# Performance work log

Measured on AMD Instinct MI355X. Metric: run time of the kernel, lower is better.

Reference implementation:

```python
import jax, jax.numpy as jnp
import numpy as np

N = 27            # hardcoded node count in the module
D = 1024          # state_dim
E = D * 5         # MHA embed dim = 5120
H = 4             # n_heads


def setup_inputs() -> dict:
    key = jax.random.key(0)
    ks = jax.random.split(key, 6)
    s = 0.02
    return {
        "node_states": jax.random.normal(ks[0], (N, D, 5), jnp.float32),
        "hist_prev": jax.random.normal(ks[1], (N, D, 5), jnp.float32),
        "granger_w": jax.random.normal(ks[2], (1, 2 * E), jnp.float32) * s,
        "granger_b": jnp.zeros((1,), jnp.float32),
        "in_proj_w": jax.random.normal(ks[3], (3 * E, E), jnp.float32) * s,
        "in_proj_b": jnp.zeros((3 * E,), jnp.float32),
        "out_proj_w": jax.random.normal(ks[4], (E, E), jnp.float32) * s,
        "out_proj_b": jnp.zeros((E,), jnp.float32),
        "light_hertz": 500,
    }


def _mha(x, in_w, in_b, out_w, out_b):
    # x: [N, E]; torch MultiheadAttention with q=k=v=x, batch of 1
    qkv = x @ in_w.T + in_b                       # [N, 3E]
    q, k, v = jnp.split(qkv, 3, axis=-1)          # each [N, E]
    hd = E // H
    q = q.reshape(N, H, hd).transpose(1, 0, 2)    # [H, N, hd]
    k = k.reshape(N, H, hd).transpose(1, 0, 2)
    v = v.reshape(N, H, hd).transpose(1, 0, 2)
    scores = jnp.einsum('hqd,hkd->hqk', q, k) / jnp.sqrt(jnp.float32(hd))
    attn = jax.nn.softmax(scores, axis=-1)        # [H, N, N]
    o = jnp.einsum('hqk,hkd->hqd', attn, v)       # [H, N, hd]
    o = o.transpose(1, 0, 2).reshape(N, E)
    return o @ out_w.T + out_b                    # [N, E]


def reference(node_states, hist_prev, granger_w, granger_b,
              in_proj_w, in_proj_b, out_proj_w, out_proj_b, light_hertz):
    node_flat = node_states.reshape(N, E)         # [N, E]
    hist_flat = hist_prev.reshape(N, E)           # [N, E]

    # Granger pairwise test, vectorized: pred_input = [hist[j], node[i]]
    # score[i, j] = sigmoid(hist[j] . w_h + node[i] . w_n + b)
    w_h = granger_w[0, :E]
    w_n = granger_w[0, E:]
    col = node_flat @ w_n                          # [N] -> varies with i
    row = hist_flat @ w_h                          # [N] -> varies with j
    adj = jax.nn.sigmoid(col[:, None] + row[None, :] + granger_b[0])  # [N, N]
    causal_adj = adj * (1.0 - jnp.eye(N, dtype=adj.dtype))            # zero diagonal

    hertz_weight = jnp.clip(jnp.float32(light_hertz) / 1000.0, 0.1, 1.0)
    attended = _mha(node_flat, in_proj_w, in_proj_b, out_proj_w, out_proj_b)
    out = (attended * hertz_weight).reshape(N, D, 5)
    return out, causal_adj
```

## Files before the change

kernel.cpp:

```cpp
#include <hip/hip_runtime.h>

#define NROW 27
#define EDIM 5120
#define QKVDIM 15360
#define HD 1280

typedef __attribute__((ext_vector_type(8))) short bf16x8;
typedef __attribute__((ext_vector_type(4))) float f32x4;

__device__ inline short f2bf(float x) {
    unsigned u = __builtin_bit_cast(unsigned, x);
    u = (u + 0x7FFFu + ((u >> 16) & 1u)) >> 16;
    return (short)u;
}
__device__ inline float bf2f(short h) {
    unsigned u = ((unsigned)(unsigned short)h) << 16;
    return __builtin_bit_cast(float, u);
}

#define KC 64
#define LDK 72

__device__ inline void loadX2(float* xbuf, const float* xp, bool xok) {
    if (xok) {
        *(float4*)&xbuf[0] = ((const float4*)xp)[0];
        *(float4*)&xbuf[4] = ((const float4*)xp)[1];
    } else {
        #pragma unroll
        for (int j = 0; j < 8; ++j) xbuf[j] = 0.f;
    }
}

__device__ inline void loadWfrag(float4* wreg, const float* wp0, const float* wp1) {
    #pragma unroll
    for (int s = 0; s < 2; ++s) {
        wreg[s * 2 + 0] = *(const float4*)(wp0 + 32 * s);
        wreg[s * 2 + 1] = *(const float4*)(wp0 + 32 * s + 4);
        wreg[4 + s * 2 + 0] = *(const float4*)(wp1 + 32 * s);
        wreg[4 + s * 2 + 1] = *(const float4*)(wp1 + 32 * s + 4);
    }
}

__global__ __launch_bounds__(256, 3)
void gemm_regw(const float* __restrict__ X, const float* __restrict__ W,
               float* __restrict__ Cp, int K, int Ntot, int Kblk)
{
    __shared__ __align__(16) short Xhi[2][32][LDK];
    __shared__ __align__(16) short Xlo[2][32][LDK];

    const int tid = threadIdx.x;
    const int n0 = blockIdx.x * 128;
    const int k0 = blockIdx.y * Kblk;

    const int lane = tid & 63;
    const int wv   = tid >> 6;
    const int lm   = lane & 15;
    const int q8   = (lane >> 4) * 8;

    f32x4 acc[2][2] = {};

    const int xr = tid >> 3;
    const int xk = (tid & 7) * 8;
    const bool xok = (xr < NROW);
    const float* xp = X + (size_t)(xok ? xr : 0) * K + k0 + xk;

    const float* wp0 = W + (size_t)(n0 + 32 * wv + lm) * K + k0 + q8;
    const float* wp1 = wp0 + (size_t)16 * K;

    float  xbuf[8];
    float4 wreg[8];

    loadX2(xbuf, xp, xok);
    loadWfrag(wreg, wp0, wp1);

    const int nc = Kblk / KC;
    int p = 0;
    for (int c = 0; c < nc; ++c) {
        {
            bf16x8 h8, l8;
            #pragma unroll
            for (int j = 0; j < 8; ++j) {
                short h = f2bf(xbuf[j]);
                h8[j] = h;
                l8[j] = f2bf(xbuf[j] - bf2f(h));
            }
            *(bf16x8*)&Xhi[p][xr][xk] = h8;
            *(bf16x8*)&Xlo[p][xr][xk] = l8;
        }

        bf16x8 whi[2][2], wlo[2][2];
        #pragma unroll
        for (int g = 0; g < 2; ++g) {
            #pragma unroll
            for (int s = 0; s < 2; ++s) {
                const float4 a = wreg[g * 4 + s * 2 + 0];
                const float4 b = wreg[g * 4 + s * 2 + 1];
                const float f[8] = {a.x, a.y, a.z, a.w, b.x, b.y, b.z, b.w};
                bf16x8 h8, l8;
                #pragma unroll
                for (int j = 0; j < 8; ++j) {
                    short h = f2bf(f[j]);
                    h8[j] = h;
                    l8[j] = f2bf(f[j] - bf2f(h));
                }
                whi[s][g] = h8;
                wlo[s][g] = l8;
            }
        }

        if (c + 1 < nc) {
            xp  += KC;
            wp0 += KC;
            wp1 += KC;
            loadX2(xbuf, xp, xok);
            loadWfrag(wreg, wp0, wp1);
        }

        __syncthreads();

        #pragma unroll
        for (int s = 0; s < 2; ++s) {
            const int ko = 32 * s + q8;
            bf16x8 ah0 = *(const bf16x8*)&Xhi[p][lm][ko];
            bf16x8 ah1 = *(const bf16x8*)&Xhi[p][lm + 16][ko];
            bf16x8 al0 = *(const bf16x8*)&Xlo[p][lm][ko];
            bf16x8 al1 = *(const bf16x8*)&Xlo[p][lm + 16][ko];

            acc[0][0] = __builtin_amdgcn_mfma_f32_16x16x32_bf16(ah0, whi[s][0], acc[0][0], 0, 0, 0);
            acc[0][0] = __builtin_amdgcn_mfma_f32_16x16x32_bf16(ah0, wlo[s][0], acc[0][0], 0, 0, 0);
            acc[0][0] = __builtin_amdgcn_mfma_f32_16x16x32_bf16(al0, whi[s][0], acc[0][0], 0, 0, 0);

            acc[0][1] = __builtin_amdgcn_mfma_f32_16x16x32_bf16(ah0, whi[s][1], acc[0][1], 0, 0, 0);
            acc[0][1] = __builtin_amdgcn_mfma_f32_16x16x32_bf16(ah0, wlo[s][1], acc[0][1], 0, 0, 0);
            acc[0][1] = __builtin_amdgcn_mfma_f32_16x16x32_bf16(al0, whi[s][1], acc[0][1], 0, 0, 0);

            acc[1][0] = __builtin_amdgcn_mfma_f32_16x16x32_bf16(ah1, whi[s][0], acc[1][0], 0, 0, 0);
            acc[1][0] = __builtin_amdgcn_mfma_f32_16x16x32_bf16(ah1, wlo[s][0], acc[1][0], 0, 0, 0);
            acc[1][0] = __builtin_amdgcn_mfma_f32_16x16x32_bf16(al1, whi[s][0], acc[1][0], 0, 0, 0);

            acc[1][1] = __builtin_amdgcn_mfma_f32_16x16x32_bf16(ah1, whi[s][1], acc[1][1], 0, 0, 0);
            acc[1][1] = __builtin_amdgcn_mfma_f32_16x16x32_bf16(ah1, wlo[s][1], acc[1][1], 0, 0, 0);
            acc[1][1] = __builtin_amdgcn_mfma_f32_16x16x32_bf16(al1, whi[s][1], acc[1][1], 0, 0, 0);
        }
        p ^= 1;
    }

    const size_t base = (size_t)blockIdx.y * NROW * Ntot;
    #pragma unroll
    for (int mi = 0; mi < 2; ++mi) {
        #pragma unroll
        for (int r = 0; r < 4; ++r) {
            const int m = mi * 16 + (lane >> 4) * 4 + r;
            if (m < NROW) {
                #pragma unroll
                for (int ni = 0; ni < 2; ++ni) {
                    const int n = n0 + 32 * wv + ni * 16 + lm;
                    Cp[base + (size_t)m * Ntot + n] = acc[mi][ni][r];
                }
            }
        }
    }
}

__global__ __launch_bounds__(256)
void reduce_kernel(const float* __restrict__ Cp, const float* __restrict__ bias,
                   float* __restrict__ out, int Ntot, int nky, const int* __restrict__ hz,
                   const float* __restrict__ cr, const float* __restrict__ gb,
                   float* __restrict__ adj)
{
    if (adj && blockIdx.x == gridDim.x - 1) {
        for (int t = threadIdx.x; t < NROW * NROW; t += 256) {
            const int i = t / NROW, j = t % NROW;
            float v = 0.f;
            if (i != j) {
                float z = cr[i] + cr[NROW + j] + gb[0];
                v = 1.0f / (1.0f + expf(-z));
            }
            adj[t] = v;
        }
        return;
    }
    const int idx = blockIdx.x * 256 + threadIdx.x;
    const int total4 = NROW * Ntot / 4;
    if (idx >= total4) return;
    float4 s = ((const float4*)Cp)[idx];
    for (int k = 1; k < nky; ++k) {
        float4 p = ((const float4*)(Cp + (size_t)k * NROW * Ntot))[idx];
        s.x += p.x; s.y += p.y; s.z += p.z; s.w += p.w;
    }
    const int n = (idx * 4) % Ntot;
    float4 b = *(const float4*)(bias + n);
    s.x += b.x; s.y += b.y; s.z += b.z; s.w += b.w;
    if (hz) {
        float h = (float)hz[0] * 0.001f;
        float sc = fminf(fmaxf(h, 0.1f), 1.0f);
        s.x *= sc; s.y *= sc; s.z *= sc; s.w *= sc;
    }
    ((float4*)out)[idx] = s;
}

__global__ __launch_bounds__(256)
void colrow_kernel(const float* __restrict__ node, const float* __restrict__ hist,
                   const float* __restrict__ gw, float* __restrict__ cr)
{
    const int b = blockIdx.x;
    const float* x = (b < NROW) ? node + (size_t)b * EDIM : hist + (size_t)(b - NROW) * EDIM;
    const float* w = (b < NROW) ? gw + EDIM : gw;
    const int tid = threadIdx.x;
    float a = 0.f;
    for (int f = tid; f < EDIM / 4; f += 256) {
        float4 xv = ((const float4*)x)[f];
        float4 wv = ((const float4*)w)[f];
        a += xv.x * wv.x + xv.y * wv.y + xv.z * wv.z + xv.w * wv.w;
    }
    #pragma unroll
    for (int off = 32; off; off >>= 1) a += __shfl_down(a, off);
    __shared__ float red[4];
    if ((tid & 63) == 0) red[tid >> 6] = a;
    __syncthreads();
    if (tid == 0) cr[b] = red[0] + red[1] + red[2] + red[3];
}

__global__ __launch_bounds__(256)
void attn_kernel(const float* __restrict__ qkv, float* __restrict__ O)
{
    __shared__ float qs[HD];
    __shared__ float sc[NROW];
    __shared__ float pr[NROW];
    const int bx = blockIdx.x;
    const int h = bx & 3;
    const int i = bx >> 2;
    const int tid = threadIdx.x;

    const size_t qoff = (size_t)i * QKVDIM + (size_t)h * HD;
    for (int d = tid; d < HD; d += 256) qs[d] = qkv[qoff + d];
    __syncthreads();

    const int wid = tid >> 6, lane = tid & 63;
    for (int j = wid; j < NROW; j += 4) {
        const float* kr = qkv + (size_t)j * QKVDIM + EDIM + (size_t)h * HD;
        float a = 0.f;
        #pragma unroll
        for (int it = 0; it < 5; ++it) {
            int d4 = lane + 64 * it;
            float4 k4 = *(const float4*)(kr + 4 * d4);
            float4 q4 = *(const float4*)(qs + 4 * d4);
            a += q4.x * k4.x + q4.y * k4.y + q4.z * k4.z + q4.w * k4.w;
        }
        #pragma unroll
        for (int off = 32; off; off >>= 1) a += __shfl_down(a, off);
        if (lane == 0) sc[j] = a * 0.02795084971874737f;
    }
    __syncthreads();

    float mxv = -1e30f;
    for (int j = 0; j < NROW; ++j) mxv = fmaxf(mxv, sc[j]);
    float s = 0.f;
    for (int j = 0; j < NROW; ++j) s += expf(sc[j] - mxv);
    if (tid < NROW) pr[tid] = expf(sc[tid] - mxv) / s;
    __syncthreads();

    for (int d4 = tid; d4 < HD / 4; d4 += 256) {
        float4 o = make_float4(0.f, 0.f, 0.f, 0.f);
        for (int j = 0; j < NROW; ++j) {
            const float4 v4 = *(const float4*)(qkv + (size_t)j * QKVDIM + 2 * EDIM + (size_t)h * HD + 4 * d4);
            const float p = pr[j];
            o.x = fmaf(p, v4.x, o.x);
            o.y = fmaf(p, v4.y, o.y);
            o.z = fmaf(p, v4.z, o.z);
            o.w = fmaf(p, v4.w, o.w);
        }
        *(float4*)(O + (size_t)i * EDIM + (size_t)h * HD + 4 * d4) = o;
    }
}

extern "C" void kernel_launch(void* const* d_in, const int* in_sizes, int n_in,
                              void* d_out, int out_size, void* d_ws, size_t ws_size,
                              hipStream_t stream)
{
    const float* node = (const float*)d_in[0];
    const float* hist = (const float*)d_in[1];
    const float* gw   = (const float*)d_in[2];
    const float* gb   = (const float*)d_in[3];
    const float* inw  = (const float*)d_in[4];
    const float* inb  = (const float*)d_in[5];
    const float* outw = (const float*)d_in[6];
    const float* outb = (const float*)d_in[7];
    const int*   hz   = (const int*)d_in[8];

    float* out = (float*)d_out;

    float* Cp1  = (float*)d_ws;
    float* qkvf = Cp1 + (size_t)8 * NROW * QKVDIM;
    float* Obuf = qkvf + (size_t)NROW * QKVDIM;
    float* Cp2  = Obuf + (size_t)NROW * EDIM;
    float* cr   = Cp2 + (size_t)16 * NROW * EDIM;

    colrow_kernel<<<54, 256, 0, stream>>>(node, hist, gw, cr);

    gemm_regw<<<dim3(120, 8), 256, 0, stream>>>(node, inw, Cp1, EDIM, QKVDIM, EDIM / 8);
    reduce_kernel<<<NROW * QKVDIM / 4 / 256, 256, 0, stream>>>(
        Cp1, inb, qkvf, QKVDIM, 8, nullptr, nullptr, nullptr, nullptr);

    attn_kernel<<<108, 256, 0, stream>>>(qkvf, Obuf);

    gemm_regw<<<dim3(40, 16), 256, 0, stream>>>(Obuf, outw, Cp2, EDIM, EDIM, EDIM / 16);
    reduce_kernel<<<NROW * EDIM / 4 / 256 + 1, 256, 0, stream>>>(
        Cp2, outb, out, EDIM, 16, hz, cr, gb, out + (size_t)NROW * EDIM);
}
```

Baseline: 534.5 us.

## Pre-split activations into bf16 hi/lo in producers and drop GEMM LDS staging

```diff
diff --git a/kernel.cpp b/kernel.cpp
--- a/kernel.cpp
+++ b/kernel.cpp
@@ -19,35 +19,86 @@
 }
 
 #define KC 64
-#define LDK 72
-
-__device__ inline void loadX2(float* xbuf, const float* xp, bool xok) {
-    if (xok) {
-        *(float4*)&xbuf[0] = ((const float4*)xp)[0];
-        *(float4*)&xbuf[4] = ((const float4*)xp)[1];
-    } else {
+
+__device__ __forceinline__ void loadW8(float4* wb, const float* wq0, const float* wq1) {
+    #pragma unroll
+    for (int s = 0; s < 2; ++s) {
+        wb[s * 2 + 0]     = *(const float4*)(wq0 + 32 * s);
+        wb[s * 2 + 1]     = *(const float4*)(wq0 + 32 * s + 4);
+        wb[4 + s * 2 + 0] = *(const float4*)(wq1 + 32 * s);
+        wb[4 + s * 2 + 1] = *(const float4*)(wq1 + 32 * s + 4);
+    }
+}
+
+__device__ __forceinline__ void gstep(
+    const short* __restrict__ xh0, const short* __restrict__ xh1,
+    const short* __restrict__ xl0, const short* __restrict__ xl1, bool xok1,
+    const float* __restrict__ wq0, const float* __restrict__ wq1,
+    int c, int nc, float4* wcur, float4* wnxt, f32x4 (&acc)[2][2])
+{
+    const int ko = c * KC;
+
+    bf16x8 ah0[2], ah1[2], al0[2], al1[2];
+    #pragma unroll
+    for (int s = 0; s < 2; ++s) {
+        ah0[s] = *(const bf16x8*)(xh0 + ko + 32 * s);
+        al0[s] = *(const bf16x8*)(xl0 + ko + 32 * s);
+        bf16x8 h1 = {}, l1 = {};
+        if (xok1) {
+            h1 = *(const bf16x8*)(xh1 + ko + 32 * s);
+            l1 = *(const bf16x8*)(xl1 + ko + 32 * s);
+        }
+        ah1[s] = h1;
+        al1[s] = l1;
+    }
+
+    if (c + 1 < nc) loadW8(wnxt, wq0 + (c + 1) * KC, wq1 + (c + 1) * KC);
+
+    bf16x8 whi[2][2], wlo[2][2];
+    #pragma unroll
+    for (int g = 0; g < 2; ++g) {
         #pragma unroll
-        for (int j = 0; j < 8; ++j) xbuf[j] = 0.f;
-    }
-}
-
-__device__ inline void loadWfrag(float4* wreg, const float* wp0, const float* wp1) {
+        for (int s = 0; s < 2; ++s) {
+            const float4 a = wcur[g * 4 + s * 2 + 0];
+            const float4 b = wcur[g * 4 + s * 2 + 1];
+            const float f[8] = {a.x, a.y, a.z, a.w, b.x, b.y, b.z, b.w};
+            bf16x8 h8, l8;
+            #pragma unroll
+            for (int j = 0; j < 8; ++j) {
+                short h = f2bf(f[j]);
+                h8[j] = h;
+                l8[j] = f2bf(f[j] - bf2f(h));
+            }
+            whi[s][g] = h8;
+            wlo[s][g] = l8;
+        }
+    }
+
     #pragma unroll
     for (int s = 0; s < 2; ++s) {
-        wreg[s * 2 + 0] = *(const float4*)(wp0 + 32 * s);
-        wreg[s * 2 + 1] = *(const float4*)(wp0 + 32 * s + 4);
-        wreg[4 + s * 2 + 0] = *(const float4*)(wp1 + 32 * s);
-        wreg[4 + s * 2 + 1] = *(const float4*)(wp1 + 32 * s + 4);
-    }
-}
-
-__global__ __launch_bounds__(256, 3)
-void gemm_regw(const float* __restrict__ X, const float* __restrict__ W,
-               float* __restrict__ Cp, int K, int Ntot, int Kblk)
-{
-    __shared__ __align__(16) short Xhi[2][32][LDK];
-    __shared__ __align__(16) short Xlo[2][32][LDK];
-
+        acc[0][0] = __builtin_amdgcn_mfma_f32_16x16x32_bf16(ah0[s], whi[s][0], acc[0][0], 0, 0, 0);
+        acc[0][0] = __builtin_amdgcn_mfma_f32_16x16x32_bf16(ah0[s], wlo[s][0], acc[0][0], 0, 0, 0);
+        acc[0][0] = __builtin_amdgcn_mfma_f32_16x16x32_bf16(al0[s], whi[s][0], acc[0][0], 0, 0, 0);
+
+        acc[0][1] = __builtin_amdgcn_mfma_f32_16x16x32_bf16(ah0[s], whi[s][1], acc[0][1], 0, 0, 0);
+        acc[0][1] = __builtin_amdgcn_mfma_f32_16x16x32_bf16(ah0[s], wlo[s][1], acc[0][1], 0, 0, 0);
+        acc[0][1] = __builtin_amdgcn_mfma_f32_16x16x32_bf16(al0[s], whi[s][1], acc[0][1], 0, 0, 0);
+
+        acc[1][0] = __builtin_amdgcn_mfma_f32_16x16x32_bf16(ah1[s], whi[s][0], acc[1][0], 0, 0, 0);
+        acc[1][0] = __builtin_amdgcn_mfma_f32_16x16x32_bf16(ah1[s], wlo[s][0], acc[1][0], 0, 0, 0);
+        acc[1][0] = __builtin_amdgcn_mfma_f32_16x16x32_bf16(al1[s], whi[s][0], acc[1][0], 0, 0, 0);
+
+        acc[1][1] = __builtin_amdgcn_mfma_f32_16x16x32_bf16(ah1[s], whi[s][1], acc[1][1], 0, 0, 0);
+        acc[1][1] = __builtin_amdgcn_mfma_f32_16x16x32_bf16(ah1[s], wlo[s][1], acc[1][1], 0, 0, 0);
+        acc[1][1] = __builtin_amdgcn_mfma_f32_16x16x32_bf16(al1[s], whi[s][1], acc[1][1], 0, 0, 0);
+    }
+}
+
+__global__ __launch_bounds__(256, 2)
+void gemm_regw(const short* __restrict__ Xhi, const short* __restrict__ Xlo,
+               const float* __restrict__ W, float* __restrict__ Cp,
+               int K, int Ntot, int Kblk)
+{
     const int tid = threadIdx.x;
     const int n0 = blockIdx.x * 128;
     const int k0 = blockIdx.y * Kblk;
@@ -59,90 +110,27 @@
 
     f32x4 acc[2][2] = {};
 
-    const int xr = tid >> 3;
-    const int xk = (tid & 7) * 8;
-    const bool xok = (xr < NROW);
-    const float* xp = X + (size_t)(xok ? xr : 0) * K + k0 + xk;
-
     const float* wp0 = W + (size_t)(n0 + 32 * wv + lm) * K + k0 + q8;
     const float* wp1 = wp0 + (size_t)16 * K;
 
-    float  xbuf[8];
-    float4 wreg[8];
-
-    loadX2(xbuf, xp, xok);
-    loadWfrag(wreg, wp0, wp1);
+    const bool xok1 = (lm + 16) < NROW;
+    const int  r1   = xok1 ? lm + 16 : 0;
+    const short* xh0 = Xhi + (size_t)lm * K + k0 + q8;
+    const short* xl0 = Xlo + (size_t)lm * K + k0 + q8;
+    const short* xh1 = Xhi + (size_t)r1 * K + k0 + q8;
+    const short* xl1 = Xlo + (size_t)r1 * K + k0 + q8;
+
+    float4 wA[8], wB[8];
+    loadW8(wA, wp0, wp1);
 
     const int nc = Kblk / KC;
-    int p = 0;
-    for (int c = 0; c < nc; ++c) {
-        {
-            bf16x8 h8, l8;
-            #pragma unroll
-            for (int j = 0; j < 8; ++j) {
-                short h = f2bf(xbuf[j]);
-                h8[j] = h;
-                l8[j] = f2bf(xbuf[j] - bf2f(h));
-            }
-            *(bf16x8*)&Xhi[p][xr][xk] = h8;
-            *(bf16x8*)&Xlo[p][xr][xk] = l8;
-        }
-
-        bf16x8 whi[2][2], wlo[2][2];
-        #pragma unroll
-        for (int g = 0; g < 2; ++g) {
-            #pragma unroll
-            for (int s = 0; s < 2; ++s) {
-                const float4 a = wreg[g * 4 + s * 2 + 0];
-                const float4 b = wreg[g * 4 + s * 2 + 1];
-                const float f[8] = {a.x, a.y, a.z, a.w, b.x, b.y, b.z, b.w};
-                bf16x8 h8, l8;
-                #pragma unroll
-                for (int j = 0; j < 8; ++j) {
-                    short h = f2bf(f[j]);
-                    h8[j] = h;
-                    l8[j] = f2bf(f[j] - bf2f(h));
-                }
-                whi[s][g] = h8;
-                wlo[s][g] = l8;
-            }
-        }
-
-        if (c + 1 < nc) {
-            xp  += KC;
-            wp0 += KC;
-            wp1 += KC;
-            loadX2(xbuf, xp, xok);
-            loadWfrag(wreg, wp0, wp1);
-        }
-
-        __syncthreads();
-
-        #pragma unroll
-        for (int s = 0; s < 2; ++s) {
-            const int ko = 32 * s + q8;
-            bf16x8 ah0 = *(const bf16x8*)&Xhi[p][lm][ko];
-            bf16x8 ah1 = *(const bf16x8*)&Xhi[p][lm + 16][ko];
-            bf16x8 al0 = *(const bf16x8*)&Xlo[p][lm][ko];
-            bf16x8 al1 = *(const bf16x8*)&Xlo[p][lm + 16][ko];
-
-            acc[0][0] = __builtin_amdgcn_mfma_f32_16x16x32_bf16(ah0, whi[s][0], acc[0][0], 0, 0, 0);
-            acc[0][0] = __builtin_amdgcn_mfma_f32_16x16x32_bf16(ah0, wlo[s][0], acc[0][0], 0, 0, 0);
-            acc[0][0] = __builtin_amdgcn_mfma_f32_16x16x32_bf16(al0, whi[s][0], acc[0][0], 0, 0, 0);
-
-            acc[0][1] = __builtin_amdgcn_mfma_f32_16x16x32_bf16(ah0, whi[s][1], acc[0][1], 0, 0, 0);
-            acc[0][1] = __builtin_amdgcn_mfma_f32_16x16x32_bf16(ah0, wlo[s][1], acc[0][1], 0, 0, 0);
-            acc[0][1] = __builtin_amdgcn_mfma_f32_16x16x32_bf16(al0, whi[s][1], acc[0][1], 0, 0, 0);
-
-            acc[1][0] = __builtin_amdgcn_mfma_f32_16x16x32_bf16(ah1, whi[s][0], acc[1][0], 0, 0, 0);
-            acc[1][0] = __builtin_amdgcn_mfma_f32_16x16x32_bf16(ah1, wlo[s][0], acc[1][0], 0, 0, 0);
-            acc[1][0] = __builtin_amdgcn_mfma_f32_16x16x32_bf16(al1, whi[s][0], acc[1][0], 0, 0, 0);
-
-            acc[1][1] = __builtin_amdgcn_mfma_f32_16x16x32_bf16(ah1, whi[s][1], acc[1][1], 0, 0, 0);
-            acc[1][1] = __builtin_amdgcn_mfma_f32_16x16x32_bf16(ah1, wlo[s][1], acc[1][1], 0, 0, 0);
-            acc[1][1] = __builtin_amdgcn_mfma_f32_16x16x32_bf16(al1, whi[s][1], acc[1][1], 0, 0, 0);
-        }
-        p ^= 1;
+    int c = 0;
+    while (c < nc) {
+        gstep(xh0, xh1, xl0, xl1, xok1, wp0, wp1, c, nc, wA, wB, acc);
+        ++c;
+        if (c >= nc) break;
+        gstep(xh0, xh1, xl0, xl1, xok1, wp0, wp1, c, nc, wB, wA, acc);
+        ++c;
     }
 
     const size_t base = (size_t)blockIdx.y * NROW * Ntot;
@@ -201,17 +189,28 @@
 
 __global__ __launch_bounds__(256)
 void colrow_kernel(const float* __restrict__ node, const float* __restrict__ hist,
-                   const float* __restrict__ gw, float* __restrict__ cr)
+                   const float* __restrict__ gw, float* __restrict__ cr,
+                   short* __restrict__ XhiG, short* __restrict__ XloG)
 {
     const int b = blockIdx.x;
-    const float* x = (b < NROW) ? node + (size_t)b * EDIM : hist + (size_t)(b - NROW) * EDIM;
-    const float* w = (b < NROW) ? gw + EDIM : gw;
+    const bool isn = (b < NROW);
+    const float* x = isn ? node + (size_t)b * EDIM : hist + (size_t)(b - NROW) * EDIM;
+    const float* w = isn ? gw + EDIM : gw;
     const int tid = threadIdx.x;
     float a = 0.f;
     for (int f = tid; f < EDIM / 4; f += 256) {
         float4 xv = ((const float4*)x)[f];
         float4 wv = ((const float4*)w)[f];
         a += xv.x * wv.x + xv.y * wv.y + xv.z * wv.z + xv.w * wv.w;
+        if (isn) {
+            short4 h4, l4;
+            h4.x = f2bf(xv.x); l4.x = f2bf(xv.x - bf2f(h4.x));
+            h4.y = f2bf(xv.y); l4.y = f2bf(xv.y - bf2f(h4.y));
+            h4.z = f2bf(xv.z); l4.z = f2bf(xv.z - bf2f(h4.z));
+            h4.w = f2bf(xv.w); l4.w = f2bf(xv.w - bf2f(h4.w));
+            *(short4*)&XhiG[(size_t)b * EDIM + 4 * f] = h4;
+            *(short4*)&XloG[(size_t)b * EDIM + 4 * f] = l4;
+        }
     }
     #pragma unroll
     for (int off = 32; off; off >>= 1) a += __shfl_down(a, off);
@@ -222,7 +221,8 @@
 }
 
 __global__ __launch_bounds__(256)
-void attn_kernel(const float* __restrict__ qkv, float* __restrict__ O)
+void attn_kernel(const float* __restrict__ qkv,
+                 short* __restrict__ Ohi, short* __restrict__ Olo)
 {
     __shared__ float qs[HD];
     __shared__ float sc[NROW];
@@ -270,7 +270,14 @@
             o.z = fmaf(p, v4.z, o.z);
             o.w = fmaf(p, v4.w, o.w);
         }
-        *(float4*)(O + (size_t)i * EDIM + (size_t)h * HD + 4 * d4) = o;
+        short4 h4, l4;
+        h4.x = f2bf(o.x); l4.x = f2bf(o.x - bf2f(h4.x));
+        h4.y = f2bf(o.y); l4.y = f2bf(o.y - bf2f(h4.y));
+        h4.z = f2bf(o.z); l4.z = f2bf(o.z - bf2f(h4.z));
+        h4.w = f2bf(o.w); l4.w = f2bf(o.w - bf2f(h4.w));
+        const size_t off = (size_t)i * EDIM + (size_t)h * HD + 4 * d4;
+        *(short4*)&Ohi[off] = h4;
+        *(short4*)&Olo[off] = l4;
     }
 }
 
@@ -292,19 +299,22 @@
 
     float* Cp1  = (float*)d_ws;
     float* qkvf = Cp1 + (size_t)8 * NROW * QKVDIM;
-    float* Obuf = qkvf + (size_t)NROW * QKVDIM;
-    float* Cp2  = Obuf + (size_t)NROW * EDIM;
+    float* Cp2  = qkvf + (size_t)NROW * QKVDIM;
     float* cr   = Cp2 + (size_t)16 * NROW * EDIM;
-
-    colrow_kernel<<<54, 256, 0, stream>>>(node, hist, gw, cr);
-
-    gemm_regw<<<dim3(120, 8), 256, 0, stream>>>(node, inw, Cp1, EDIM, QKVDIM, EDIM / 8);
+    short* XhiG = (short*)(cr + 64);
+    short* XloG = XhiG + (size_t)NROW * EDIM;
+    short* OhiG = XloG + (size_t)NROW * EDIM;
+    short* OloG = OhiG + (size_t)NROW * EDIM;
+
+    colrow_kernel<<<54, 256, 0, stream>>>(node, hist, gw, cr, XhiG, XloG);
+
+    gemm_regw<<<dim3(120, 8), 256, 0, stream>>>(XhiG, XloG, inw, Cp1, EDIM, QKVDIM, EDIM / 8);
     reduce_kernel<<<NROW * QKVDIM / 4 / 256, 256, 0, stream>>>(
         Cp1, inb, qkvf, QKVDIM, 8, nullptr, nullptr, nullptr, nullptr);
 
-    attn_kernel<<<108, 256, 0, stream>>>(qkvf, Obuf);
-
-    gemm_regw<<<dim3(40, 16), 256, 0, stream>>>(Obuf, outw, Cp2, EDIM, EDIM, EDIM / 16);
+    attn_kernel<<<108, 256, 0, stream>>>(qkvf, OhiG, OloG);
+
+    gemm_regw<<<dim3(40, 16), 256, 0, stream>>>(OhiG, OloG, outw, Cp2, EDIM, EDIM, EDIM / 16);
     reduce_kernel<<<NROW * EDIM / 4 / 256 + 1, 256, 0, stream>>>(
         Cp2, outb, out, EDIM, 16, hz, cr, gb, out + (size_t)NROW * EDIM);
 }
```

Result: slower. 556.1 us (+4.0%).
